# Kernel optimization log

Hardware: AMD Instinct MI355X
Metric: run time of the kernel (lower is better)

Reference implementation:

```python
import jax, jax.numpy as jnp
import numpy as np

B, M, N, D, NH, DH = 2, 2048, 2048, 1024, 16, 64
STD = 0.02

def setup_inputs() -> dict:
    key = jax.random.key(0)
    ks = jax.random.split(key, 7)
    query = jax.random.normal(ks[0], (B, M, D), dtype=jnp.float32)
    key_value = jax.random.normal(ks[1], (B, N, D), dtype=jnp.float32)
    key_padding_mask = jax.random.uniform(ks[2], (B, N)) < 0.1
    # torch Linear weight is (out,in); store as (in,out) for x @ W
    W_Q = STD * jax.random.truncated_normal(ks[3], -2.0, 2.0, (D, NH * DH), dtype=jnp.float32)
    W_K = STD * jax.random.truncated_normal(ks[4], -2.0, 2.0, (D, NH * DH), dtype=jnp.float32)
    W_V = STD * jax.random.truncated_normal(ks[5], -2.0, 2.0, (D, NH * DH), dtype=jnp.float32)
    W_O = STD * jax.random.truncated_normal(ks[6], -2.0, 2.0, (NH * DH, D), dtype=jnp.float32)
    return {"query": query, "key_value": key_value, "key_padding_mask": key_padding_mask,
            "W_Q": W_Q, "W_K": W_K, "W_V": W_V, "W_O": W_O}

def reference(query, key_value, key_padding_mask, W_Q, W_K, W_V, W_O):
    scale = 1.0 / jnp.sqrt(jnp.float32(DH))
    Q = (query @ W_Q).reshape(B, M, NH, DH)       # (B,M,H,dh)
    K = (key_value @ W_K).reshape(B, N, NH, DH)   # (B,N,H,dh)
    V = (key_value @ W_V).reshape(B, N, NH, DH)
    scores = jnp.einsum('bmhd,bnhd->bhmn', Q, K) * scale  # (B,H,M,N)
    scores = jnp.where(key_padding_mask[:, None, None, :], -jnp.inf, scores)
    attn = jax.nn.softmax(scores, axis=-1)
    out = jnp.einsum('bhmn,bnhd->bmhd', attn, V).reshape(B, M, NH * DH)
    return out @ W_O
```

## Files before the change

### kernel.cpp

```cpp
#include <hip/hip_runtime.h>
#include <math.h>

#define BB 2
#define SEQ 2048
#define DMODEL 1024
#define NHH 16
#define DHH 64

typedef __bf16 bf16;
typedef __attribute__((ext_vector_type(8))) __bf16 bf16x8;
typedef __attribute__((ext_vector_type(4))) float f32x4;

#define C1f 0.18033688011112042f
#define C2f -5.770780163555854f

__device__ __forceinline__ void gl_lds16(const bf16* g, bf16* l) {
  __builtin_amdgcn_global_load_lds(
      (const __attribute__((address_space(1))) void*)g,
      (__attribute__((address_space(3))) void*)l, 16, 0, 0);
}

__global__ __launch_bounds__(256) void cvt2_bf16(const float* __restrict__ in0,
                                                 bf16* __restrict__ out0,
                                                 const float* __restrict__ in1,
                                                 bf16* __restrict__ out1, int n8) {
  int i = blockIdx.x * 256 + threadIdx.x;
  if (i >= n8) return;
  const float* in = blockIdx.y ? in1 : in0;
  bf16* out = blockIdx.y ? out1 : out0;
  const float4* p = (const float4*)in + 2 * (size_t)i;
  float4 a = p[0], b = p[1];
  bf16x8 v;
  v[0] = (bf16)a.x; v[1] = (bf16)a.y; v[2] = (bf16)a.z; v[3] = (bf16)a.w;
  v[4] = (bf16)b.x; v[5] = (bf16)b.y; v[6] = (bf16)b.z; v[7] = (bf16)b.w;
  *((bf16x8*)out + i) = v;
}

__global__ __launch_bounds__(256) void wt_cvt(const float* __restrict__ W0, const float* __restrict__ W1,
                                              const float* __restrict__ W2, const float* __restrict__ W3,
                                              bf16* __restrict__ O0, bf16* __restrict__ O1,
                                              bf16* __restrict__ O2, bf16* __restrict__ O3) {
  __shared__ bf16 T[64][72];
  const float* W; bf16* O;
  switch (blockIdx.z) {
    case 0: W = W0; O = O0; break;
    case 1: W = W1; O = O1; break;
    case 2: W = W2; O = O2; break;
    default: W = W3; O = O3; break;
  }
  const int n0 = blockIdx.x * 64, k0 = blockIdx.y * 64;
  const int t = threadIdx.x;
  {
    int k = t >> 2, ns = (t & 3) * 16;
    const float* g = W + (size_t)(k0 + k) * DMODEL + n0 + ns;
#pragma unroll
    for (int q = 0; q < 4; ++q) {
      float4 f = *(const float4*)(g + 4 * q);
      T[ns + 4 * q + 0][k] = (bf16)f.x;
      T[ns + 4 * q + 1][k] = (bf16)f.y;
      T[ns + 4 * q + 2][k] = (bf16)f.z;
      T[ns + 4 * q + 3][k] = (bf16)f.w;
    }
  }
  __syncthreads();
  {
    int n = t >> 2, ks = (t & 3) * 16;
    bf16x8 a = *(const bf16x8*)&T[n][ks];
    bf16x8 b = *(const bf16x8*)&T[n][ks + 8];
    bf16* o = O + (size_t)(n0 + n) * DMODEL + k0 + ks;
    *(bf16x8*)o = a;
    *(bf16x8*)(o + 8) = b;
  }
}

template <bool F32OUT>
__device__ __forceinline__ void gemm128_body(const bf16* __restrict__ A,
                                             const bf16* __restrict__ Bt,
                                             float* __restrict__ Cf,
                                             bf16* __restrict__ Cb,
                                             bf16* As0, bf16* Bs0,
                                             bf16* As1, bf16* Bs1) {
  const int t = threadIdx.x;
  const int lane = t & 63, wave = t >> 6;
  const int l15 = lane & 15, quad = lane >> 4;
  const int bm = blockIdx.y * 128, bn = blockIdx.x * 128;
  const int wr = wave >> 1, wc = wave & 1;

  const int srow = wave * 32 + (lane >> 3);
  const int sc = lane & 7;
  const int ca = sc ^ ((lane >> 3) & 7);
  const bf16* gA = A + (size_t)(bm + srow) * DMODEL + ca * 8;
  const bf16* gB = Bt + (size_t)(bn + srow) * DMODEL + ca * 8;
  const int lo = wave * 32 * 64;

  f32x4 acc[4][4] = {};

#define STAGE(KT, AS, BS)                                              \
  {                                                                    \
    const int kk = (KT) * 64;                                          \
    _Pragma("unroll") for (int j = 0; j < 4; ++j) {                    \
      gl_lds16(gA + (size_t)(j * 8) * DMODEL + kk, (AS) + lo + j * 512); \
      gl_lds16(gB + (size_t)(j * 8) * DMODEL + kk, (BS) + lo + j * 512); \
    }                                                                  \
  }

#define COMPUTE(AS, BS)                                                \
  {                                                                    \
    _Pragma("unroll") for (int ks = 0; ks < 2; ++ks) {                 \
      bf16x8 af[4], bfr[4];                                            \
      _Pragma("unroll") for (int mt = 0; mt < 4; ++mt) {               \
        int row = wr * 64 + mt * 16 + l15;                             \
        int s = (ks * 4 + quad) ^ (row & 7);                           \
        af[mt] = *(const bf16x8*)&(AS)[row * 64 + s * 8];              \
      }                                                                \
      _Pragma("unroll") for (int nt = 0; nt < 4; ++nt) {               \
        int row = wc * 64 + nt * 16 + l15;                             \
        int s = (ks * 4 + quad) ^ (row & 7);                           \
        bfr[nt] = *(const bf16x8*)&(BS)[row * 64 + s * 8];             \
      }                                                                \
      _Pragma("unroll") for (int mt = 0; mt < 4; ++mt)                 \
          _Pragma("unroll") for (int nt = 0; nt < 4; ++nt)             \
              acc[mt][nt] = __builtin_amdgcn_mfma_f32_16x16x32_bf16(   \
                  af[mt], bfr[nt], acc[mt][nt], 0, 0, 0);              \
    }                                                                  \
  }

  STAGE(0, As0, Bs0);
  __syncthreads();

  for (int kt = 0; kt < DMODEL / 64; kt += 2) {
    if (kt + 1 < DMODEL / 64) STAGE(kt + 1, As1, Bs1);
    COMPUTE(As0, Bs0);
    __syncthreads();
    if (kt + 2 < DMODEL / 64) STAGE(kt + 2, As0, Bs0);
    COMPUTE(As1, Bs1);
    __syncthreads();
  }
#undef STAGE
#undef COMPUTE

#pragma unroll
  for (int mt = 0; mt < 4; ++mt)
#pragma unroll
    for (int nt = 0; nt < 4; ++nt)
#pragma unroll
      for (int r = 0; r < 4; ++r) {
        int row = bm + wr * 64 + mt * 16 + quad * 4 + r;
        int col = bn + wc * 64 + nt * 16 + l15;
        if (F32OUT) Cf[(size_t)row * DMODEL + col] = acc[mt][nt][r];
        else Cb[(size_t)row * DMODEL + col] = (bf16)acc[mt][nt][r];
      }
}

__global__ __launch_bounds__(256, 2) void gemm_qkv(const bf16* __restrict__ qbf,
                                                   const bf16* __restrict__ kvbf,
                                                   const bf16* __restrict__ WtQ,
                                                   const bf16* __restrict__ WtK,
                                                   const bf16* __restrict__ WtV,
                                                   bf16* __restrict__ Qb,
                                                   bf16* __restrict__ Kb,
                                                   bf16* __restrict__ Vb) {
  __shared__ bf16 As0[128 * 64], Bs0[128 * 64];
  __shared__ bf16 As1[128 * 64], Bs1[128 * 64];
  const bf16 *A, *Bt; bf16* C;
  switch (blockIdx.z) {
    case 0: A = qbf; Bt = WtQ; C = Qb; break;
    case 1: A = kvbf; Bt = WtK; C = Kb; break;
    default: A = kvbf; Bt = WtV; C = Vb; break;
  }
  gemm128_body<false>(A, Bt, nullptr, C, As0, Bs0, As1, Bs1);
}

__global__ __launch_bounds__(256, 2) void gemm_out(const bf16* __restrict__ A,
                                                   const bf16* __restrict__ Wt,
                                                   float* __restrict__ C) {
  __shared__ bf16 As0[128 * 64], Bs0[128 * 64];
  __shared__ bf16 As1[128 * 64], Bs1[128 * 64];
  gemm128_body<true>(A, Wt, C, nullptr, As0, Bs0, As1, Bs1);
}

__global__ __launch_bounds__(256) void attn_mfma(const bf16* __restrict__ Qb,
                                                 const bf16* __restrict__ Kb,
                                                 const bf16* __restrict__ Vb,
                                                 const int* __restrict__ maskp,
                                                 bf16* __restrict__ Ob) {
  __shared__ bf16 Ks[2][64 * 64];
  __shared__ bf16 Vt[2][64][68];
  __shared__ bf16 Ps[4][32][36];
  __shared__ bf16 msk01[2][64];

  const int blk = blockIdx.x;
  const int h = blk & 15;
  const int b = (blk >> 4) & 1;
  const int qb = blk >> 5;
  const int t = threadIdx.x;
  const int wave = t >> 6, lane = t & 63;
  const int l15 = lane & 15, quad = lane >> 4;
  bf16(*PsW)[36] = Ps[wave];

  const int kr = t >> 2, kq = t & 3;
  const bf16* gK = Kb + (size_t)(b * SEQ + kr) * DMODEL + h * 64 + kq * 16;
  const int s0 = (kq * 2) ^ (kr & 7), s1 = (kq * 2 + 1) ^ (kr & 7);
  const int nv = (t & 31) * 2, dc = (t >> 5) * 8;
  const bf16* gV = Vb + (size_t)(b * SEQ + nv) * DMODEL + h * 64 + dc;
  const int* gM = maskp + b * SEQ;

  {
    bf16x8 k0 = *(const bf16x8*)(gK);
    bf16x8 k1 = *(const bf16x8*)(gK + 8);
    bf16x8 v0 = *(const bf16x8*)(gV);
    bf16x8 v1 = *(const bf16x8*)(gV + DMODEL);
    int2 m2 = *(const int2*)(gM + nv);
    *(bf16x8*)&Ks[0][kr * 64 + s0 * 8] = k0;
    *(bf16x8*)&Ks[0][kr * 64 + s1 * 8] = k1;
    union U { bf16x8 v; uint32_t dw[4]; } a, c;
    a.v = v0; c.v = v1;
    const uint32_t zA = m2.x ? 0u : 0xFFFFFFFFu;
    const uint32_t zB = m2.y ? 0u : 0xFFFFFFFFu;
#pragma unroll
    for (int d2 = 0; d2 < 4; ++d2) {
      uint32_t A0 = a.dw[d2] & zA, B0 = c.dw[d2] & zB;
      *(uint32_t*)&Vt[0][dc + 2 * d2 + 0][nv] = __builtin_amdgcn_perm(B0, A0, 0x05040100u);
      *(uint32_t*)&Vt[0][dc + 2 * d2 + 1][nv] = __builtin_amdgcn_perm(B0, A0, 0x07060302u);
    }
    if (t < 64) msk01[0][t] = gM[t] ? (bf16)0.f : (bf16)1.f;
  }

  bf16x8 qf[2][2];
#pragma unroll
  for (int mt = 0; mt < 2; ++mt)
#pragma unroll
    for (int ks = 0; ks < 2; ++ks) {
      const bf16* g = Qb + (size_t)(b * SEQ + qb * 128 + wave * 32 + mt * 16 + l15) * DMODEL +
                      h * 64 + ks * 32 + quad * 8;
      qf[mt][ks] = *(const bf16x8*)g;
    }

  f32x4 o[2][4] = {};
  f32x4 acc_l[2] = {};

  __syncthreads();

  for (int it = 0; it < SEQ / 64; ++it) {
    const int p = it & 1;
    const bool more = (it + 1) < SEQ / 64;
    bf16x8 kreg0, kreg1, vreg0, vreg1;
    int2 vm;
    int mreg = 0;
    if (more) {
      const int nn = (it + 1) * 64;
      const bf16* gK2 = gK + (size_t)nn * DMODEL;
      const bf16* gV2 = gV + (size_t)nn * DMODEL;
      kreg0 = *(const bf16x8*)(gK2);
      kreg1 = *(const bf16x8*)(gK2 + 8);
      vreg0 = *(const bf16x8*)(gV2);
      vreg1 = *(const bf16x8*)(gV2 + DMODEL);
      vm = *(const int2*)(gM + nn + nv);
      if (t < 64) mreg = gM[nn + t];
    }

    f32x4 s[2][4] = {};
#pragma unroll
    for (int ks = 0; ks < 2; ++ks) {
      bf16x8 kf[4];
#pragma unroll
      for (int nt = 0; nt < 4; ++nt) {
        int row = nt * 16 + l15;
        int sl = (ks * 4 + quad) ^ (row & 7);
        kf[nt] = *(const bf16x8*)&Ks[p][row * 64 + sl * 8];
      }
#pragma unroll
      for (int mt = 0; mt < 2; ++mt)
#pragma unroll
        for (int nt = 0; nt < 4; ++nt)
          s[mt][nt] = __builtin_amdgcn_mfma_f32_16x16x32_bf16(qf[mt][ks], kf[nt], s[mt][nt], 0, 0, 0);
    }

#pragma unroll
    for (int ks2 = 0; ks2 < 2; ++ks2) {
#pragma unroll
      for (int mt = 0; mt < 2; ++mt)
#pragma unroll
        for (int nt2 = 0; nt2 < 2; ++nt2)
#pragma unroll
          for (int r = 0; r < 4; ++r) {
            float pex = __builtin_amdgcn_exp2f(s[mt][ks2 * 2 + nt2][r] * C1f + C2f);
            PsW[mt * 16 + quad * 4 + r][nt2 * 16 + l15] = (bf16)pex;
          }
      bf16x8 pa[2], vb[4];
#pragma unroll
      for (int mt = 0; mt < 2; ++mt)
        pa[mt] = *(const bf16x8*)&PsW[mt * 16 + l15][quad * 8];
#pragma unroll
      for (int dt = 0; dt < 4; ++dt)
        vb[dt] = *(const bf16x8*)&Vt[p][dt * 16 + l15][ks2 * 32 + quad * 8];
      union OU { bf16x8 v; uint32_t dw[4]; } of;
      of.v = *(const bf16x8*)&msk01[p][ks2 * 32 + quad * 8];
      const uint32_t zc = (l15 == 0) ? 0xFFFFFFFFu : 0u;
#pragma unroll
      for (int d = 0; d < 4; ++d) of.dw[d] &= zc;
#pragma unroll
      for (int mt = 0; mt < 2; ++mt) {
#pragma unroll
        for (int dt = 0; dt < 4; ++dt)
          o[mt][dt] = __builtin_amdgcn_mfma_f32_16x16x32_bf16(pa[mt], vb[dt], o[mt][dt], 0, 0, 0);
        acc_l[mt] = __builtin_amdgcn_mfma_f32_16x16x32_bf16(pa[mt], of.v, acc_l[mt], 0, 0, 0);
      }
    }

    if (more) {
      const int q = 1 - p;
      *(bf16x8*)&Ks[q][kr * 64 + s0 * 8] = kreg0;
      *(bf16x8*)&Ks[q][kr * 64 + s1 * 8] = kreg1;
      union U { bf16x8 v; uint32_t dw[4]; } a, c;
      a.v = vreg0; c.v = vreg1;
      const uint32_t zA = vm.x ? 0u : 0xFFFFFFFFu;
      const uint32_t zB = vm.y ? 0u : 0xFFFFFFFFu;
#pragma unroll
      for (int d2 = 0; d2 < 4; ++d2) {
        uint32_t A0 = a.dw[d2] & zA, B0 = c.dw[d2] & zB;
        *(uint32_t*)&Vt[q][dc + 2 * d2 + 0][nv] = __builtin_amdgcn_perm(B0, A0, 0x05040100u);
        *(uint32_t*)&Vt[q][dc + 2 * d2 + 1][nv] = __builtin_amdgcn_perm(B0, A0, 0x07060302u);
      }
      if (t < 64) msk01[q][t] = mreg ? (bf16)0.f : (bf16)1.f;
    }
    __syncthreads();
  }

#pragma unroll
  for (int mt = 0; mt < 2; ++mt)
#pragma unroll
    for (int r = 0; r < 4; ++r) {
      float lv = __shfl(acc_l[mt][r], lane & 48);
      float inv = 1.f / lv;
      int row = b * SEQ + qb * 128 + wave * 32 + mt * 16 + quad * 4 + r;
#pragma unroll
      for (int dt = 0; dt < 4; ++dt) {
        int col = h * 64 + dt * 16 + l15;
        Ob[(size_t)row * DMODEL + col] = (bf16)(o[mt][dt][r] * inv);
      }
    }
}

extern "C" void kernel_launch(void* const* d_in, const int* in_sizes, int n_in,
                              void* d_out, int out_size, void* d_ws, size_t ws_size,
                              hipStream_t stream) {
  (void)in_sizes; (void)n_in; (void)out_size; (void)ws_size;
  const float* query = (const float*)d_in[0];
  const float* key_value = (const float*)d_in[1];
  const int* mask = (const int*)d_in[2];
  const float* W_Q = (const float*)d_in[3];
  const float* W_K = (const float*)d_in[4];
  const float* W_V = (const float*)d_in[5];
  const float* W_O = (const float*)d_in[6];
  float* out = (float*)d_out;

  const size_t TOK = (size_t)BB * SEQ;
  const size_t TE = TOK * DMODEL;
  char* w = (char*)d_ws;
  bf16* qbf = (bf16*)w;   w += TE * 2;
  bf16* kvbf = (bf16*)w;  w += TE * 2;
  bf16* WtQ = (bf16*)w;   w += (size_t)DMODEL * DMODEL * 2;
  bf16* WtK = (bf16*)w;   w += (size_t)DMODEL * DMODEL * 2;
  bf16* WtV = (bf16*)w;   w += (size_t)DMODEL * DMODEL * 2;
  bf16* WtO = (bf16*)w;   w += (size_t)DMODEL * DMODEL * 2;
  bf16* Qbuf = (bf16*)w;  w += TE * 2;
  bf16* Kbuf = (bf16*)w;  w += TE * 2;
  bf16* Vbuf = (bf16*)w;  w += TE * 2;
  bf16* Obuf = (bf16*)w;  w += TE * 2;

  cvt2_bf16<<<dim3(TE / 8 / 256, 2), 256, 0, stream>>>(query, qbf, key_value, kvbf, TE / 8);
  wt_cvt<<<dim3(16, 16, 4), 256, 0, stream>>>(W_Q, W_K, W_V, W_O, WtQ, WtK, WtV, WtO);

  gemm_qkv<<<dim3(DMODEL / 128, TOK / 128, 3), 256, 0, stream>>>(qbf, kvbf, WtQ, WtK, WtV,
                                                                 Qbuf, Kbuf, Vbuf);

  attn_mfma<<<BB * NHH * (SEQ / 128), 256, 0, stream>>>(Qbuf, Kbuf, Vbuf, mask, Obuf);

  gemm_out<<<dim3(DMODEL / 128, TOK / 128), 256, 0, stream>>>(Obuf, WtO, out);
}
```

Before: 238.7 us.

## Rewrite attention with 32x32 MFMA, register-resident P, and fuse prep kernels

The attention kernel now computes transposed scores (K·Qᵀ) with 32x32x16 MFMAs so the exponentiated probabilities stay in registers. They are packed to bf16 and rearranged with permlane32 swaps to feed the PV MFMA directly, which removes the per-wave LDS staging of P. Masking moves from zeroing V rows plus an extra MFMA for the row sum to a ballot bitmask applied to P, with the sum accumulated in scalar registers. The two conversion kernels are merged into one launch, and output is written as packed bf16 vectors. This relies on inline asm for gfx950 instructions and a more intricate lane mapping.

```diff
diff --git a/kernel.cpp b/kernel.cpp
--- a/kernel.cpp
+++ b/kernel.cpp
@@ -10,9 +10,19 @@
 typedef __bf16 bf16;
 typedef __attribute__((ext_vector_type(8))) __bf16 bf16x8;
 typedef __attribute__((ext_vector_type(4))) float f32x4;
+typedef __attribute__((ext_vector_type(16))) float f32x16;
 
 #define C1f 0.18033688011112042f
 #define C2f -5.770780163555854f
+
+__device__ __forceinline__ uint32_t cvtpk_bf16(float lo, float hi) {
+  uint32_t r;
+  asm("v_cvt_pk_bf16_f32 %0, %1, %2" : "=v"(r) : "v"(lo), "v"(hi));
+  return r;
+}
+__device__ __forceinline__ void pl32swap(uint32_t& a, uint32_t& b) {
+  asm("v_permlane32_swap_b32 %0, %1" : "+v"(a), "+v"(b));
+}
 
 __device__ __forceinline__ void gl_lds16(const bf16* g, bf16* l) {
   __builtin_amdgcn_global_load_lds(
@@ -20,36 +30,38 @@
       (__attribute__((address_space(3))) void*)l, 16, 0, 0);
 }
 
-__global__ __launch_bounds__(256) void cvt2_bf16(const float* __restrict__ in0,
-                                                 bf16* __restrict__ out0,
-                                                 const float* __restrict__ in1,
-                                                 bf16* __restrict__ out1, int n8) {
-  int i = blockIdx.x * 256 + threadIdx.x;
-  if (i >= n8) return;
-  const float* in = blockIdx.y ? in1 : in0;
-  bf16* out = blockIdx.y ? out1 : out0;
-  const float4* p = (const float4*)in + 2 * (size_t)i;
-  float4 a = p[0], b = p[1];
-  bf16x8 v;
-  v[0] = (bf16)a.x; v[1] = (bf16)a.y; v[2] = (bf16)a.z; v[3] = (bf16)a.w;
-  v[4] = (bf16)b.x; v[5] = (bf16)b.y; v[6] = (bf16)b.z; v[7] = (bf16)b.w;
-  *((bf16x8*)out + i) = v;
-}
-
-__global__ __launch_bounds__(256) void wt_cvt(const float* __restrict__ W0, const float* __restrict__ W1,
-                                              const float* __restrict__ W2, const float* __restrict__ W3,
-                                              bf16* __restrict__ O0, bf16* __restrict__ O1,
-                                              bf16* __restrict__ O2, bf16* __restrict__ O3) {
+__global__ __launch_bounds__(256) void prep(const float* __restrict__ query,
+                                            const float* __restrict__ key_value,
+                                            bf16* __restrict__ qbf,
+                                            bf16* __restrict__ kvbf,
+                                            const float* __restrict__ W0, const float* __restrict__ W1,
+                                            const float* __restrict__ W2, const float* __restrict__ W3,
+                                            bf16* __restrict__ O0, bf16* __restrict__ O1,
+                                            bf16* __restrict__ O2, bf16* __restrict__ O3) {
   __shared__ bf16 T[64][72];
+  const int bid = blockIdx.x;
+  const int t = threadIdx.x;
+  if (bid >= 1024) {
+    const int bidc = bid - 1024;
+    const float* in = (bidc >> 11) ? key_value : query;
+    bf16* out = (bidc >> 11) ? kvbf : qbf;
+    const int i = (bidc & 2047) * 256 + t;
+    const float4* p = (const float4*)in + 2 * (size_t)i;
+    float4 a = p[0], b = p[1];
+    bf16x8 v;
+    v[0] = (bf16)a.x; v[1] = (bf16)a.y; v[2] = (bf16)a.z; v[3] = (bf16)a.w;
+    v[4] = (bf16)b.x; v[5] = (bf16)b.y; v[6] = (bf16)b.z; v[7] = (bf16)b.w;
+    *((bf16x8*)out + i) = v;
+    return;
+  }
   const float* W; bf16* O;
-  switch (blockIdx.z) {
+  switch (bid >> 8) {
     case 0: W = W0; O = O0; break;
     case 1: W = W1; O = O1; break;
     case 2: W = W2; O = O2; break;
     default: W = W3; O = O3; break;
   }
-  const int n0 = blockIdx.x * 64, k0 = blockIdx.y * 64;
-  const int t = threadIdx.x;
+  const int n0 = (bid & 15) * 64, k0 = ((bid >> 4) & 15) * 64;
   {
     int k = t >> 2, ns = (t & 3) * 16;
     const float* g = W + (size_t)(k0 + k) * DMODEL + n0 + ns;
@@ -95,13 +107,13 @@
 
   f32x4 acc[4][4] = {};
 
-#define STAGE(KT, AS, BS)                                              \
-  {                                                                    \
-    const int kk = (KT) * 64;                                          \
-    _Pragma("unroll") for (int j = 0; j < 4; ++j) {                    \
+#define STAGE(KT, AS, BS)                                                \
+  {                                                                      \
+    const int kk = (KT) * 64;                                            \
+    _Pragma("unroll") for (int j = 0; j < 4; ++j) {                      \
       gl_lds16(gA + (size_t)(j * 8) * DMODEL + kk, (AS) + lo + j * 512); \
       gl_lds16(gB + (size_t)(j * 8) * DMODEL + kk, (BS) + lo + j * 512); \
-    }                                                                  \
+    }                                                                    \
   }
 
 #define COMPUTE(AS, BS)                                                \
@@ -186,8 +198,6 @@
                                                  bf16* __restrict__ Ob) {
   __shared__ bf16 Ks[2][64 * 64];
   __shared__ bf16 Vt[2][64][68];
-  __shared__ bf16 Ps[4][32][36];
-  __shared__ bf16 msk01[2][64];
 
   const int blk = blockIdx.x;
   const int h = blk & 15;
@@ -195,8 +205,7 @@
   const int qb = blk >> 5;
   const int t = threadIdx.x;
   const int wave = t >> 6, lane = t & 63;
-  const int l15 = lane & 15, quad = lane >> 4;
-  bf16(*PsW)[36] = Ps[wave];
+  const int l31 = lane & 31, hi = lane >> 5;
 
   const int kr = t >> 2, kq = t & 3;
   const bf16* gK = Kb + (size_t)(b * SEQ + kr) * DMODEL + h * 64 + kq * 16;
@@ -208,45 +217,39 @@
   {
     bf16x8 k0 = *(const bf16x8*)(gK);
     bf16x8 k1 = *(const bf16x8*)(gK + 8);
+    *(bf16x8*)&Ks[0][kr * 64 + s0 * 8] = k0;
+    *(bf16x8*)&Ks[0][kr * 64 + s1 * 8] = k1;
     bf16x8 v0 = *(const bf16x8*)(gV);
     bf16x8 v1 = *(const bf16x8*)(gV + DMODEL);
-    int2 m2 = *(const int2*)(gM + nv);
-    *(bf16x8*)&Ks[0][kr * 64 + s0 * 8] = k0;
-    *(bf16x8*)&Ks[0][kr * 64 + s1 * 8] = k1;
     union U { bf16x8 v; uint32_t dw[4]; } a, c;
     a.v = v0; c.v = v1;
-    const uint32_t zA = m2.x ? 0u : 0xFFFFFFFFu;
-    const uint32_t zB = m2.y ? 0u : 0xFFFFFFFFu;
 #pragma unroll
     for (int d2 = 0; d2 < 4; ++d2) {
-      uint32_t A0 = a.dw[d2] & zA, B0 = c.dw[d2] & zB;
-      *(uint32_t*)&Vt[0][dc + 2 * d2 + 0][nv] = __builtin_amdgcn_perm(B0, A0, 0x05040100u);
-      *(uint32_t*)&Vt[0][dc + 2 * d2 + 1][nv] = __builtin_amdgcn_perm(B0, A0, 0x07060302u);
-    }
-    if (t < 64) msk01[0][t] = gM[t] ? (bf16)0.f : (bf16)1.f;
-  }
-
-  bf16x8 qf[2][2];
-#pragma unroll
-  for (int mt = 0; mt < 2; ++mt)
-#pragma unroll
-    for (int ks = 0; ks < 2; ++ks) {
-      const bf16* g = Qb + (size_t)(b * SEQ + qb * 128 + wave * 32 + mt * 16 + l15) * DMODEL +
-                      h * 64 + ks * 32 + quad * 8;
-      qf[mt][ks] = *(const bf16x8*)g;
-    }
-
-  f32x4 o[2][4] = {};
-  f32x4 acc_l[2] = {};
+      *(uint32_t*)&Vt[0][dc + 2 * d2 + 0][nv] = __builtin_amdgcn_perm(c.dw[d2], a.dw[d2], 0x05040100u);
+      *(uint32_t*)&Vt[0][dc + 2 * d2 + 1][nv] = __builtin_amdgcn_perm(c.dw[d2], a.dw[d2], 0x07060302u);
+    }
+  }
+  int mcur = gM[lane];
+
+  bf16x8 qf[4];
+#pragma unroll
+  for (int ks = 0; ks < 4; ++ks) {
+    const bf16* g = Qb + (size_t)(b * SEQ + qb * 128 + wave * 32 + l31) * DMODEL +
+                    h * 64 + ks * 16 + hi * 8;
+    qf[ks] = *(const bf16x8*)g;
+  }
+
+  f32x16 o0 = {}, o1 = {};
+  float lsum = 0.f;
 
   __syncthreads();
 
   for (int it = 0; it < SEQ / 64; ++it) {
     const int p = it & 1;
     const bool more = (it + 1) < SEQ / 64;
+
     bf16x8 kreg0, kreg1, vreg0, vreg1;
-    int2 vm;
-    int mreg = 0;
+    int mnext = 0;
     if (more) {
       const int nn = (it + 1) * 64;
       const bf16* gK2 = gK + (size_t)nn * DMODEL;
@@ -255,56 +258,55 @@
       kreg1 = *(const bf16x8*)(gK2 + 8);
       vreg0 = *(const bf16x8*)(gV2);
       vreg1 = *(const bf16x8*)(gV2 + DMODEL);
-      vm = *(const int2*)(gM + nn + nv);
-      if (t < 64) mreg = gM[nn + t];
-    }
-
-    f32x4 s[2][4] = {};
-#pragma unroll
-    for (int ks = 0; ks < 2; ++ks) {
-      bf16x8 kf[4];
-#pragma unroll
-      for (int nt = 0; nt < 4; ++nt) {
-        int row = nt * 16 + l15;
-        int sl = (ks * 4 + quad) ^ (row & 7);
-        kf[nt] = *(const bf16x8*)&Ks[p][row * 64 + sl * 8];
+      mnext = gM[nn + lane];
+    }
+
+    f32x16 s0v = {}, s1v = {};
+#pragma unroll
+    for (int ks = 0; ks < 4; ++ks) {
+      const int c = ks * 2 + hi;
+      const int r0 = l31;
+      const int r1 = 32 + l31;
+      bf16x8 ka0 = *(const bf16x8*)&Ks[p][r0 * 64 + (c ^ (r0 & 7)) * 8];
+      bf16x8 ka1 = *(const bf16x8*)&Ks[p][r1 * 64 + (c ^ (r1 & 7)) * 8];
+      s0v = __builtin_amdgcn_mfma_f32_32x32x16_bf16(ka0, qf[ks], s0v, 0, 0, 0);
+      s1v = __builtin_amdgcn_mfma_f32_32x32x16_bf16(ka1, qf[ks], s1v, 0, 0, 0);
+    }
+
+    const unsigned long long mb = __ballot(mcur == 0);
+
+#pragma unroll
+    for (int kt = 0; kt < 2; ++kt) {
+      const f32x16 sv = kt ? s1v : s0v;
+      const uint32_t ml = (uint32_t)(mb >> (kt * 32 + 4 * hi));
+      float pm[16];
+#pragma unroll
+      for (int r = 0; r < 16; ++r) {
+        const int bitc = (r & 3) + 8 * (r >> 2);
+        float pex = __builtin_amdgcn_exp2f(sv[r] * C1f + C2f);
+        pm[r] = ((ml >> bitc) & 1u) ? pex : 0.f;
+        lsum += pm[r];
       }
-#pragma unroll
-      for (int mt = 0; mt < 2; ++mt)
-#pragma unroll
-        for (int nt = 0; nt < 4; ++nt)
-          s[mt][nt] = __builtin_amdgcn_mfma_f32_16x16x32_bf16(qf[mt][ks], kf[nt], s[mt][nt], 0, 0, 0);
-    }
-
-#pragma unroll
-    for (int ks2 = 0; ks2 < 2; ++ks2) {
-#pragma unroll
-      for (int mt = 0; mt < 2; ++mt)
-#pragma unroll
-        for (int nt2 = 0; nt2 < 2; ++nt2)
-#pragma unroll
-          for (int r = 0; r < 4; ++r) {
-            float pex = __builtin_amdgcn_exp2f(s[mt][ks2 * 2 + nt2][r] * C1f + C2f);
-            PsW[mt * 16 + quad * 4 + r][nt2 * 16 + l15] = (bf16)pex;
-          }
-      bf16x8 pa[2], vb[4];
-#pragma unroll
-      for (int mt = 0; mt < 2; ++mt)
-        pa[mt] = *(const bf16x8*)&PsW[mt * 16 + l15][quad * 8];
-#pragma unroll
-      for (int dt = 0; dt < 4; ++dt)
-        vb[dt] = *(const bf16x8*)&Vt[p][dt * 16 + l15][ks2 * 32 + quad * 8];
-      union OU { bf16x8 v; uint32_t dw[4]; } of;
-      of.v = *(const bf16x8*)&msk01[p][ks2 * 32 + quad * 8];
-      const uint32_t zc = (l15 == 0) ? 0xFFFFFFFFu : 0u;
-#pragma unroll
-      for (int d = 0; d < 4; ++d) of.dw[d] &= zc;
-#pragma unroll
-      for (int mt = 0; mt < 2; ++mt) {
-#pragma unroll
-        for (int dt = 0; dt < 4; ++dt)
-          o[mt][dt] = __builtin_amdgcn_mfma_f32_16x16x32_bf16(pa[mt], vb[dt], o[mt][dt], 0, 0, 0);
-        acc_l[mt] = __builtin_amdgcn_mfma_f32_16x16x32_bf16(pa[mt], of.v, acc_l[mt], 0, 0, 0);
+      uint32_t w01 = cvtpk_bf16(pm[0], pm[1]),  w23 = cvtpk_bf16(pm[2], pm[3]);
+      uint32_t w45 = cvtpk_bf16(pm[4], pm[5]),  w67 = cvtpk_bf16(pm[6], pm[7]);
+      uint32_t w89 = cvtpk_bf16(pm[8], pm[9]),  wab = cvtpk_bf16(pm[10], pm[11]);
+      uint32_t wcd = cvtpk_bf16(pm[12], pm[13]), wef = cvtpk_bf16(pm[14], pm[15]);
+      pl32swap(w01, w45);
+      pl32swap(w23, w67);
+      pl32swap(w89, wcd);
+      pl32swap(wab, wef);
+      union BF { uint32_t u[4]; bf16x8 v; } f0, f1;
+      f0.u[0] = w01; f0.u[1] = w23; f0.u[2] = w45; f0.u[3] = w67;
+      f1.u[0] = w89; f1.u[1] = wab; f1.u[2] = wcd; f1.u[3] = wef;
+      {
+        bf16x8 va00 = *(const bf16x8*)&Vt[p][0 + l31][(kt * 2 + 0) * 16 + hi * 8];
+        bf16x8 va01 = *(const bf16x8*)&Vt[p][0 + l31][(kt * 2 + 1) * 16 + hi * 8];
+        o0 = __builtin_amdgcn_mfma_f32_32x32x16_bf16(va00, f0.v, o0, 0, 0, 0);
+        o0 = __builtin_amdgcn_mfma_f32_32x32x16_bf16(va01, f1.v, o0, 0, 0, 0);
+        bf16x8 va10 = *(const bf16x8*)&Vt[p][32 + l31][(kt * 2 + 0) * 16 + hi * 8];
+        bf16x8 va11 = *(const bf16x8*)&Vt[p][32 + l31][(kt * 2 + 1) * 16 + hi * 8];
+        o1 = __builtin_amdgcn_mfma_f32_32x32x16_bf16(va10, f0.v, o1, 0, 0, 0);
+        o1 = __builtin_amdgcn_mfma_f32_32x32x16_bf16(va11, f1.v, o1, 0, 0, 0);
       }
     }
 
@@ -314,32 +316,29 @@
       *(bf16x8*)&Ks[q][kr * 64 + s1 * 8] = kreg1;
       union U { bf16x8 v; uint32_t dw[4]; } a, c;
       a.v = vreg0; c.v = vreg1;
-      const uint32_t zA = vm.x ? 0u : 0xFFFFFFFFu;
-      const uint32_t zB = vm.y ? 0u : 0xFFFFFFFFu;
 #pragma unroll
       for (int d2 = 0; d2 < 4; ++d2) {
-        uint32_t A0 = a.dw[d2] & zA, B0 = c.dw[d2] & zB;
-        *(uint32_t*)&Vt[q][dc + 2 * d2 + 0][nv] = __builtin_amdgcn_perm(B0, A0, 0x05040100u);
-        *(uint32_t*)&Vt[q][dc + 2 * d2 + 1][nv] = __builtin_amdgcn_perm(B0, A0, 0x07060302u);
+        *(uint32_t*)&Vt[q][dc + 2 * d2 + 0][nv] = __builtin_amdgcn_perm(c.dw[d2], a.dw[d2], 0x05040100u);
+        *(uint32_t*)&Vt[q][dc + 2 * d2 + 1][nv] = __builtin_amdgcn_perm(c.dw[d2], a.dw[d2], 0x07060302u);
       }
-      if (t < 64) msk01[q][t] = mreg ? (bf16)0.f : (bf16)1.f;
-    }
+    }
+    mcur = mnext;
     __syncthreads();
   }
 
-#pragma unroll
-  for (int mt = 0; mt < 2; ++mt)
-#pragma unroll
-    for (int r = 0; r < 4; ++r) {
-      float lv = __shfl(acc_l[mt][r], lane & 48);
-      float inv = 1.f / lv;
-      int row = b * SEQ + qb * 128 + wave * 32 + mt * 16 + quad * 4 + r;
-#pragma unroll
-      for (int dt = 0; dt < 4; ++dt) {
-        int col = h * 64 + dt * 16 + l15;
-        Ob[(size_t)row * DMODEL + col] = (bf16)(o[mt][dt][r] * inv);
-      }
-    }
+  const float lt = lsum + __shfl_xor(lsum, 32);
+  const float inv = 1.f / lt;
+  bf16* gO = Ob + (size_t)(b * SEQ + qb * 128 + wave * 32 + l31) * DMODEL + h * 64;
+#pragma unroll
+  for (int g = 0; g < 4; ++g) {
+    uint2 st0, st1;
+    st0.x = cvtpk_bf16(o0[4 * g + 0] * inv, o0[4 * g + 1] * inv);
+    st0.y = cvtpk_bf16(o0[4 * g + 2] * inv, o0[4 * g + 3] * inv);
+    st1.x = cvtpk_bf16(o1[4 * g + 0] * inv, o1[4 * g + 1] * inv);
+    st1.y = cvtpk_bf16(o1[4 * g + 2] * inv, o1[4 * g + 3] * inv);
+    *(uint2*)(gO + 8 * g + 4 * hi) = st0;
+    *(uint2*)(gO + 32 + 8 * g + 4 * hi) = st1;
+  }
 }
 
 extern "C" void kernel_launch(void* const* d_in, const int* in_sizes, int n_in,
@@ -369,8 +368,8 @@
   bf16* Vbuf = (bf16*)w;  w += TE * 2;
   bf16* Obuf = (bf16*)w;  w += TE * 2;
 
-  cvt2_bf16<<<dim3(TE / 8 / 256, 2), 256, 0, stream>>>(query, qbf, key_value, kvbf, TE / 8);
-  wt_cvt<<<dim3(16, 16, 4), 256, 0, stream>>>(W_Q, W_K, W_V, W_O, WtQ, WtK, WtV, WtO);
+  prep<<<5120, 256, 0, stream>>>(query, key_value, qbf, kvbf,
+                                 W_Q, W_K, W_V, W_O, WtQ, WtK, WtV, WtO);
 
   gemm_qkv<<<dim3(DMODEL / 128, TOK / 128, 3), 256, 0, stream>>>(qbf, kvbf, WtQ, WtK, WtV,
                                                                  Qbuf, Kbuf, Vbuf);
```

Result: faster. 212.5 us (-10.9%).
